# Optimization experiments

Hardware: AMD Instinct MI355X
Metric: run time of the kernel (lower is better)

The kernel has to match this reference:

```python
import jax, jax.numpy as jnp
import numpy as np
from jax import lax

SIGMOID_THRESH = 0.05  # hard-coded in get_local_max_coords
KERNEL = 3             # default kernel_size


def setup_inputs() -> dict:
    key = jax.random.key(0)
    # [B, num_kps, H, W] heatmap logits from the DeepLab head
    heatmaps = jax.random.normal(key, (16, 17, 384, 384), dtype=jnp.float32)
    return {"heatmaps": heatmaps}


def reference(heatmaps):
    """CenterNet-style local-max peak extraction.

    Faithful to Heatmaps.get_local_max_coords: a pixel is a peak iff it equals
    the 3x3 max-pool of the logits AND sigmoid(logit) > 0.05. Instead of the
    data-dependent torch.nonzero + Python grouping loops (which just reshuffle
    the same information into ragged per-image/per-type lists), we return the
    dense, fixed-shape peak-score map: sigmoid(logit) at peak locations, 0
    elsewhere. The [B, K, H, W] layout already encodes the per-image (axis 0)
    and per-keypoint-type (axis 1) grouping of the original nested loops.
    """
    # 3x3 max-pool, stride 1, SAME padding (pad = kernel // 2)
    max_hm = lax.reduce_window(
        heatmaps,
        -jnp.inf,
        lax.max,
        window_dimensions=(1, 1, KERNEL, KERNEL),
        window_strides=(1, 1, 1, 1),
        padding="SAME",
    )
    prob = jax.nn.sigmoid(heatmaps)
    peak_mask = (max_hm == heatmaps) & (prob > SIGMOID_THRESH)
    return jnp.where(peak_mask, prob, jnp.zeros((), dtype=heatmaps.dtype))
```

## Files before the change

kernel.cpp:

```cpp
#include <hip/hip_runtime.h>
#include <math.h>

#define HH 384
#define WW 384
#define TW 64
#define TH 64
#define TX 6
#define TY 6
#define NIMG 272
#define IMG_STRIDE (HH * WW)
#define LDS_W 67
#define NELEM (66 * 66)
#define NLOAD 18

typedef float f4_t __attribute__((ext_vector_type(4)));

__device__ __forceinline__ float max3f(float a, float b, float c) {
    return fmaxf(fmaxf(a, b), c);
}
__device__ __forceinline__ float fast_sigmoid(float v) {
    return __fdividef(1.0f, 1.0f + __expf(-v));
}

__global__ __launch_bounds__(256) void
heatmap_peaks_kernel(const float* __restrict__ in, float* __restrict__ out) {
    __shared__ float S[66 * LDS_W];

    int tid = threadIdx.x;
    int bid = blockIdx.x;
    int txt = bid % TX;
    int tmp = bid / TX;
    int tyt = tmp % TY;
    int img = tmp / TY;
    int x0 = txt * TW;
    int y0 = tyt * TH;

    const float* ib = in + (size_t)img * IMG_STRIDE;
    const float NEG = -INFINITY;

    float va[NLOAD];
    bool  ok[NLOAD];
    int   le[NLOAD];
#pragma unroll
    for (int k = 0; k < NLOAD; ++k) {
        int e  = tid + k * 256;
        int ly = e / 66;
        int lx = e - ly * 66;
        int gx = x0 - 1 + lx;
        int gy = y0 - 1 + ly;
        bool valid = (e < NELEM) && ((unsigned)gx < (unsigned)WW)
                                 && ((unsigned)gy < (unsigned)HH);
        int cx = valid ? gx : 0;
        int cy = valid ? gy : 0;
        va[k] = ib[cy * WW + cx];
        ok[k] = valid;
        le[k] = ly * LDS_W + lx;
    }
#pragma unroll
    for (int k = 0; k < NLOAD; ++k) {
        int e = tid + k * 256;
        if (e < NELEM) S[le[k]] = ok[k] ? va[k] : NEG;
    }
    __syncthreads();

    int ctx = tid & 15;
    int cty = tid >> 4;
    int rb  = cty * 4;
    int cb  = ctx * 4;

    float vals[6][6];
#pragma unroll
    for (int c = 0; c < 6; ++c)
#pragma unroll
        for (int r = 0; r < 6; ++r)
            vals[c][r] = S[(rb + r) * LDS_W + cb + c];

    float vm[6][4];
#pragma unroll
    for (int c = 0; c < 6; ++c)
#pragma unroll
        for (int r = 0; r < 4; ++r)
            vm[c][r] = max3f(vals[c][r], vals[c][r + 1], vals[c][r + 2]);

    float* ob = out + (size_t)img * IMG_STRIDE
                    + (size_t)(y0 + rb) * WW + x0 + cb;
#pragma unroll
    for (int r = 0; r < 4; ++r) {
        f4_t o;
        float p, m, v;
        m = max3f(vm[0][r], vm[1][r], vm[2][r]); v = vals[1][r + 1];
        p = fast_sigmoid(v); o.x = (m == v && p > 0.05f) ? p : 0.0f;
        m = max3f(vm[1][r], vm[2][r], vm[3][r]); v = vals[2][r + 1];
        p = fast_sigmoid(v); o.y = (m == v && p > 0.05f) ? p : 0.0f;
        m = max3f(vm[2][r], vm[3][r], vm[4][r]); v = vals[3][r + 1];
        p = fast_sigmoid(v); o.z = (m == v && p > 0.05f) ? p : 0.0f;
        m = max3f(vm[3][r], vm[4][r], vm[5][r]); v = vals[4][r + 1];
        p = fast_sigmoid(v); o.w = (m == v && p > 0.05f) ? p : 0.0f;
        __builtin_nontemporal_store(o, (f4_t*)(ob + (size_t)r * WW));
    }
}

extern "C" void kernel_launch(void* const* d_in, const int* in_sizes, int n_in,
                              void* d_out, int out_size, void* d_ws, size_t ws_size,
                              hipStream_t stream) {
    const float* in = (const float*)d_in[0];
    float* out = (float*)d_out;
    int blocks = TX * TY * NIMG;
    heatmap_peaks_kernel<<<blocks, 256, 0, stream>>>(in, out);
}
```

Before: 266.7 us.

## Replace LDS-tiled stencil with per-thread vertical row streaming and XCD swizzle

Drops the shared-memory 66x66 tile load and the barrier. Each thread now owns a 4-wide column strip of 16 rows and streams rows through a rolling window of horizontal maxima held in registers. Neighbour columns are read directly from global memory and are expected to hit in cache, and the block index is swizzled across the 8 XCDs for locality. Halo reads per strip are only 2 rows instead of a 2-pixel border, at the cost of redundant scalar left/right loads per row.

```diff
diff --git a/kernel.cpp b/kernel.cpp
--- a/kernel.cpp
+++ b/kernel.cpp
@@ -3,15 +3,16 @@
 
 #define HH 384
 #define WW 384
-#define TW 64
-#define TH 64
-#define TX 6
-#define TY 6
 #define NIMG 272
 #define IMG_STRIDE (HH * WW)
-#define LDS_W 67
-#define NELEM (66 * 66)
-#define NLOAD 18
+#define ROWS 16
+#define STRIPS (HH / ROWS)
+#define C4N (WW / 4)
+#define UNITS_PER_IMG (C4N * STRIPS)
+#define TOTAL_UNITS (UNITS_PER_IMG * NIMG)
+#define BLOCK 256
+#define NBLOCKS (TOTAL_UNITS / BLOCK)
+#define NXCD 8
 
 typedef float f4_t __attribute__((ext_vector_type(4)));
 
@@ -22,81 +23,99 @@
     return __fdividef(1.0f, 1.0f + __expf(-v));
 }
 
-__global__ __launch_bounds__(256) void
-heatmap_peaks_kernel(const float* __restrict__ in, float* __restrict__ out) {
-    __shared__ float S[66 * LDS_W];
+__global__ __launch_bounds__(BLOCK) void
+heatmap_peaks_stream(const float* __restrict__ in, float* __restrict__ out) {
+    const float NEG = -INFINITY;
+    const f4_t NEG4 = {NEG, NEG, NEG, NEG};
 
-    int tid = threadIdx.x;
     int bid = blockIdx.x;
-    int txt = bid % TX;
-    int tmp = bid / TX;
-    int tyt = tmp % TY;
-    int img = tmp / TY;
-    int x0 = txt * TW;
-    int y0 = tyt * TH;
+    int swz = (bid % NXCD) * (NBLOCKS / NXCD) + bid / NXCD;
 
-    const float* ib = in + (size_t)img * IMG_STRIDE;
-    const float NEG = -INFINITY;
+    int u   = swz * BLOCK + (int)threadIdx.x;
+    int c4  = u % C4N;
+    int t   = u / C4N;
+    int s   = t % STRIPS;
+    int img = t / STRIPS;
+    int y0  = s * ROWS;
 
-    float va[NLOAD];
-    bool  ok[NLOAD];
-    int   le[NLOAD];
-#pragma unroll
-    for (int k = 0; k < NLOAD; ++k) {
-        int e  = tid + k * 256;
-        int ly = e / 66;
-        int lx = e - ly * 66;
-        int gx = x0 - 1 + lx;
-        int gy = y0 - 1 + ly;
-        bool valid = (e < NELEM) && ((unsigned)gx < (unsigned)WW)
-                                 && ((unsigned)gy < (unsigned)HH);
-        int cx = valid ? gx : 0;
-        int cy = valid ? gy : 0;
-        va[k] = ib[cy * WW + cx];
-        ok[k] = valid;
-        le[k] = ly * LDS_W + lx;
+    const float* ib = in  + (size_t)img * IMG_STRIDE + c4 * 4;
+    float*       ob = out + (size_t)img * IMG_STRIDE + (size_t)y0 * WW + c4 * 4;
+
+    const bool has_l = (c4 > 0);
+    const bool has_r = (c4 < C4N - 1);
+    const int  loff  = has_l ? -1 : 0;
+    const int  roff  = has_r ?  4 : 3;
+
+    auto ldrow = [&](int gy, f4_t& v, float& l, float& r) {
+        const float* p = ib + (size_t)gy * WW;
+        v = *(const f4_t*)p;
+        float lv = p[loff];
+        float rv = p[roff];
+        l = has_l ? lv : NEG;
+        r = has_r ? rv : NEG;
+    };
+    auto hmax = [&](f4_t v, float l, float r) -> f4_t {
+        f4_t h;
+        h.x = max3f(l,   v.x, v.y);
+        h.y = max3f(v.x, v.y, v.z);
+        h.z = max3f(v.y, v.z, v.w);
+        h.w = max3f(v.z, v.w, r);
+        return h;
+    };
+    auto emit = [&](int j, f4_t v, f4_t a, f4_t b, f4_t c) {
+        f4_t o; float m, pp;
+        m = max3f(a.x, b.x, c.x); pp = fast_sigmoid(v.x);
+        o.x = (m == v.x && pp > 0.05f) ? pp : 0.0f;
+        m = max3f(a.y, b.y, c.y); pp = fast_sigmoid(v.y);
+        o.y = (m == v.y && pp > 0.05f) ? pp : 0.0f;
+        m = max3f(a.z, b.z, c.z); pp = fast_sigmoid(v.z);
+        o.z = (m == v.z && pp > 0.05f) ? pp : 0.0f;
+        m = max3f(a.w, b.w, c.w); pp = fast_sigmoid(v.w);
+        o.w = (m == v.w && pp > 0.05f) ? pp : 0.0f;
+        __builtin_nontemporal_store(o, (f4_t*)(ob + (size_t)j * WW));
+    };
+
+    f4_t hm_prev, hm_cur, val_cur;
+
+    {
+        f4_t v; float l, r;
+        int gy = (y0 > 0) ? y0 - 1 : 0;
+        ldrow(gy, v, l, r);
+        if (y0 == 0) { v = NEG4; l = NEG; r = NEG; }
+        hm_prev = hmax(v, l, r);
     }
-#pragma unroll
-    for (int k = 0; k < NLOAD; ++k) {
-        int e = tid + k * 256;
-        if (e < NELEM) S[le[k]] = ok[k] ? va[k] : NEG;
+    {
+        f4_t v; float l, r;
+        ldrow(y0, v, l, r);
+        hm_cur  = hmax(v, l, r);
+        val_cur = v;
     }
-    __syncthreads();
+    f4_t vA; float lA, rA;
+    ldrow(y0 + 1, vA, lA, rA);
 
-    int ctx = tid & 15;
-    int cty = tid >> 4;
-    int rb  = cty * 4;
-    int cb  = ctx * 4;
-
-    float vals[6][6];
-#pragma unroll
-    for (int c = 0; c < 6; ++c)
-#pragma unroll
-        for (int r = 0; r < 6; ++r)
-            vals[c][r] = S[(rb + r) * LDS_W + cb + c];
-
-    float vm[6][4];
-#pragma unroll
-    for (int c = 0; c < 6; ++c)
-#pragma unroll
-        for (int r = 0; r < 4; ++r)
-            vm[c][r] = max3f(vals[c][r], vals[c][r + 1], vals[c][r + 2]);
-
-    float* ob = out + (size_t)img * IMG_STRIDE
-                    + (size_t)(y0 + rb) * WW + x0 + cb;
-#pragma unroll
-    for (int r = 0; r < 4; ++r) {
-        f4_t o;
-        float p, m, v;
-        m = max3f(vm[0][r], vm[1][r], vm[2][r]); v = vals[1][r + 1];
-        p = fast_sigmoid(v); o.x = (m == v && p > 0.05f) ? p : 0.0f;
-        m = max3f(vm[1][r], vm[2][r], vm[3][r]); v = vals[2][r + 1];
-        p = fast_sigmoid(v); o.y = (m == v && p > 0.05f) ? p : 0.0f;
-        m = max3f(vm[2][r], vm[3][r], vm[4][r]); v = vals[3][r + 1];
-        p = fast_sigmoid(v); o.z = (m == v && p > 0.05f) ? p : 0.0f;
-        m = max3f(vm[3][r], vm[4][r], vm[5][r]); v = vals[4][r + 1];
-        p = fast_sigmoid(v); o.w = (m == v && p > 0.05f) ? p : 0.0f;
-        __builtin_nontemporal_store(o, (f4_t*)(ob + (size_t)r * WW));
+#pragma unroll 4
+    for (int j = 0; j <= ROWS - 3; ++j) {
+        f4_t vB; float lB, rB;
+        ldrow(y0 + j + 2, vB, lB, rB);
+        f4_t hm_next = hmax(vA, lA, rA);
+        emit(j, val_cur, hm_prev, hm_cur, hm_next);
+        hm_prev = hm_cur; hm_cur = hm_next; val_cur = vA;
+        vA = vB; lA = lB; rA = rB;
+    }
+    {
+        f4_t vB; float lB, rB;
+        bool valid = (y0 + ROWS < HH);
+        int gy = valid ? y0 + ROWS : HH - 1;
+        ldrow(gy, vB, lB, rB);
+        if (!valid) { vB = NEG4; lB = NEG; rB = NEG; }
+        f4_t hm_next = hmax(vA, lA, rA);
+        emit(ROWS - 2, val_cur, hm_prev, hm_cur, hm_next);
+        hm_prev = hm_cur; hm_cur = hm_next; val_cur = vA;
+        vA = vB; lA = lB; rA = rB;
+    }
+    {
+        f4_t hm_next = hmax(vA, lA, rA);
+        emit(ROWS - 1, val_cur, hm_prev, hm_cur, hm_next);
     }
 }
 
@@ -105,6 +124,5 @@
                               hipStream_t stream) {
     const float* in = (const float*)d_in[0];
     float* out = (float*)d_out;
-    int blocks = TX * TY * NIMG;
-    heatmap_peaks_kernel<<<blocks, 256, 0, stream>>>(in, out);
+    heatmap_peaks_stream<<<NBLOCKS, BLOCK, 0, stream>>>(in, out);
 }
```

After: 279.8 us. 4.9% more time.
